# Performance work log

Hardware: AMD Instinct MI355X
Metric: run time of the kernel (lower is better)

Reference implementation:

```python
import jax, jax.numpy as jnp
import numpy as np

T, B, DIN, D = 512, 64, 1024, 1024


def setup_inputs() -> dict:
    key = jax.random.key(0)
    ks = jax.random.split(key, 11)
    s = 0.02
    inp = {
        "batch": jax.random.normal(ks[0], (T, B, DIN), dtype=jnp.float32),
        "lengths": jax.random.randint(ks[1], (B,), 0, T).astype(jnp.int32),
        "c0": jnp.zeros((D,), dtype=jnp.float32),
    }
    # gate weights stored [in, out] so application is x @ W + b
    for n, (kw, kb) in zip(["i", "f", "c", "o"], [(ks[2], ks[3]), (ks[4], ks[5]), (ks[6], ks[7]), (ks[8], ks[9])]):
        inp[f"W_{n}_w"] = jax.random.normal(kw, (DIN + D, D), dtype=jnp.float32) * s
        inp[f"W_{n}_b"] = jax.random.normal(kb, (D,), dtype=jnp.float32) * s
    return inp


def reference(batch, lengths, c0, W_i_w, W_i_b, W_f_w, W_f_b, W_c_w, W_c_b, W_o_w, W_o_b):
    Tn, Bn, _ = batch.shape
    c_init = jnp.broadcast_to(c0, (Bn, c0.shape[0]))
    h_init = jnp.tanh(c_init)
    # mask[t, b] = True where step t is past sequence b's length -> h zeroed
    mask = jnp.arange(Tn, dtype=lengths.dtype)[:, None] >= lengths[None, :]  # [T, B]

    def step(carry, xm):
        h, c = carry
        x_t, m_t = xm
        x = jnp.concatenate([x_t, h], axis=1)  # [B, DIN+D]
        i = jax.nn.sigmoid(x @ W_i_w + W_i_b)
        f = jax.nn.sigmoid(x @ W_f_w + W_f_b)
        g = jnp.tanh(x @ W_c_w + W_c_b)
        o = jax.nn.sigmoid(x @ W_o_w + W_o_b)
        c = f * c + i * g
        h = o * jnp.tanh(c)
        # in the original, new_output[mask]=0 mutates h in-place, so masked h
        # is carried into the next step's state as well as emitted as output
        h = jnp.where(m_t[:, None], jnp.zeros_like(h), h)
        return (h, c), h

    _, outs = jax.lax.scan(step, (h_init, c_init), (batch, mask))
    return outs  # [T, B, D]
```

## Files before the change

### kernel.cpp

```cpp
#include <hip/hip_runtime.h>
#include <cstddef>

typedef _Float16 f16;
typedef _Float16 f16x8 __attribute__((ext_vector_type(8)));
typedef _Float16 f16x4 __attribute__((ext_vector_type(4)));
typedef float f32x4 __attribute__((ext_vector_type(4)));

#define T_STEPS 512
#define BATCH   64
#define DD      1024
#define NTOT    4096


#define RSTRIDE_B 139264ull
#define RSTRIDE_H 69632ull
#define GSLAB_H   16384ull

#define OFF_FLAGS 0ull
#define OFF_BIAS  16384ull
#define OFF_WHP   32768ull
#define OFF_BXP   (OFF_WHP + 8388608ull)
#define OFF_XW    (OFF_BXP + 8388608ull)
#define XW_END    (OFF_XW + 268435456ull)
#define OFF_RING  XW_END
#define RING_END  (OFF_RING + 512ull * RSTRIDE_B)


__device__ __forceinline__ float sigm(float x) { return 1.f / (1.f + __expf(-x)); }
__device__ __forceinline__ float tanh_fast(float x) {
    float e = __expf(-2.f * fabsf(x));
    float t = (1.f - e) / (1.f + e);
    return x >= 0.f ? t : -t;
}

__device__ __forceinline__ unsigned int load_coh_u32(const unsigned int* p) {
    return __hip_atomic_load((unsigned int*)p, __ATOMIC_RELAXED, __HIP_MEMORY_SCOPE_AGENT);
}
__device__ __forceinline__ void store_coh_u32(unsigned int* p, unsigned int v) {
    __hip_atomic_store(p, v, __ATOMIC_RELAXED, __HIP_MEMORY_SCOPE_AGENT);
}
__device__ __forceinline__ void store_coh_u64(unsigned long long* p, unsigned long long v) {
    __hip_atomic_store(p, v, __ATOMIC_RELAXED, __HIP_MEMORY_SCOPE_AGENT);
}
__device__ __forceinline__ void waitcnt_vm0() {
    asm volatile("s_waitcnt vmcnt(0)" ::: "memory");
}

#define GATE4(g4, x0, x1, x2, x3, cvar, hvar)                        \
    {                                                                \
        float pi = (g4).x + (float)(x0);                             \
        float pf = (g4).y + (float)(x1);                             \
        float pg = (g4).z + (float)(x2);                             \
        float po = (g4).w + (float)(x3);                             \
        float iv = sigm(pi), fv = sigm(pf);                          \
        float gg = tanh_fast(pg), ov = sigm(po);                     \
        cvar = fv * cvar + iv * gg;                                  \
        hvar = ov * tanh_fast(cvar);                                 \
    }

__global__ void prepack_kernel(const float* __restrict__ Wi, const float* __restrict__ Wf,
                               const float* __restrict__ Wc, const float* __restrict__ Wo,
                               const float* __restrict__ bi, const float* __restrict__ bf,
                               const float* __restrict__ bc, const float* __restrict__ bo,
                               const float* __restrict__ c0,
                               f16* __restrict__ whp, f16* __restrict__ bxp,
                               float* __restrict__ biasp, f16* __restrict__ ring0,
                               unsigned int* __restrict__ flags)
{
    unsigned int gid = blockIdx.x * 256u + threadIdx.x;
    if (gid < 4096u) flags[gid] = 0u;
    const float* Ww[4] = {Wi, Wf, Wc, Wo};
    if (gid < 8388608u) {
        unsigned int hi = (gid >= 4194304u);
        unsigned int e  = gid & 4194303u;
        unsigned int jj = e & 7u;
        unsigned int lidx = (e >> 3) & 63u;
        unsigned int S  = (e >> 9) & 31u;
        unsigned int NT = e >> 14;
        unsigned int n  = NT * 16u + (lidx & 15u);
        unsigned int k  = S * 32u + (lidx >> 4) * 8u + jj + (hi ? 1024u : 0u);
        unsigned int g  = n & 3u, d = n >> 2;
        float v = Ww[g][k * 1024u + d];
        (hi ? whp : bxp)[e] = (f16)v;
    } else if (gid < 8392704u) {
        unsigned int n = gid - 8388608u;
        const float* Bb[4] = {bi, bf, bc, bo};
        biasp[n] = Bb[n & 3u][n >> 2];
    } else if (gid < 8458240u) {
        unsigned int e2 = gid - 8392704u;
        ring0[e2] = (f16)tanh_fast(c0[e2 & 1023u]);
    }
}

__global__ __launch_bounds__(256) void gemm_x_kernel(
    const float* __restrict__ A, const f16* __restrict__ Bp,
    const float* __restrict__ biasp, f16* __restrict__ xw)
{
    const int tid = threadIdx.x;
    const int w = tid >> 6, l = tid & 63;
    const int lr = l & 15, lq = l >> 4;
    const int n0 = blockIdx.x * 128;
    const int m0 = blockIdx.y * 128;

    f32x4 acc[2][8];
#pragma unroll
    for (int mt = 0; mt < 2; mt++)
#pragma unroll
        for (int nt = 0; nt < 8; nt++) acc[mt][nt] = (f32x4){0.f, 0.f, 0.f, 0.f};

    const float* a0 = A + (size_t)(m0 + 32 * w + lr) * 1024 + lq * 8;
    const f16x8* bp = (const f16x8*)Bp + (size_t)(n0 >> 4) * (32 * 64) + l;

#pragma unroll 2
    for (int s = 0; s < 32; s++) {
        f16x8 af[2];
#pragma unroll
        for (int mt = 0; mt < 2; mt++) {
            const float* ap = a0 + mt * (16 * 1024) + 32 * s;
            float4 v0 = *(const float4*)ap;
            float4 v1 = *(const float4*)(ap + 4);
            f16x8 tt;
            tt[0] = (f16)v0.x; tt[1] = (f16)v0.y; tt[2] = (f16)v0.z; tt[3] = (f16)v0.w;
            tt[4] = (f16)v1.x; tt[5] = (f16)v1.y; tt[6] = (f16)v1.z; tt[7] = (f16)v1.w;
            af[mt] = tt;
        }
#pragma unroll
        for (int nt = 0; nt < 8; nt++) {
            f16x8 bfr = bp[(size_t)(nt * 32 + s) * 64];
            acc[0][nt] = __builtin_amdgcn_mfma_f32_16x16x32_f16(af[0], bfr, acc[0][nt], 0, 0, 0);
            acc[1][nt] = __builtin_amdgcn_mfma_f32_16x16x32_f16(af[1], bfr, acc[1][nt], 0, 0, 0);
        }
    }
#pragma unroll
    for (int nt = 0; nt < 8; nt++) {
        int n = n0 + nt * 16 + lr;
        float bias = biasp[n];
#pragma unroll
        for (int mt = 0; mt < 2; mt++) {
#pragma unroll
            for (int r = 0; r < 4; r++) {
                int m = m0 + 32 * w + mt * 16 + lq * 4 + r;
                xw[(size_t)m * NTOT + n] = (f16)(acc[mt][nt][r] + bias);
            }
        }
    }
}

__global__ __launch_bounds__(256, 1) void lstm_persist_ring(
    const f16* __restrict__ xw, const f16* __restrict__ whp,
    const int* __restrict__ lengths, const float* __restrict__ c0,
    float* __restrict__ out, f16* ring, unsigned int* flags)
{
    extern __shared__ __align__(16) char smem[];
    f16*   wlds    = (f16*)smem;
    float* pre_lds = (float*)(smem + 131072);

    const int g  = blockIdx.x & 3;
    const int j2 = blockIdx.x >> 2;
    const int tid = threadIdx.x;
    const int wv = tid >> 6, l = tid & 63;
    const int lr = l & 15, lq = l >> 4;

    {
        const f16x8* wp = (const f16x8*)whp + (size_t)(4 * j2) * 2048;
        f16x8* wl0 = (f16x8*)wlds;
        for (int i = tid; i < 8192; i += 256) wl0[i] = wp[i];
    }
    __syncthreads();

    const int koff = lq * 8;
    const f16x8* wl = (const f16x8*)wlds + wv * 2048 + l;

    unsigned int* myflag = flags + (unsigned int)g * 1024u + (unsigned int)j2 * 16u;
    unsigned int* gflags = flags + (unsigned int)g * 1024u;

    const int b_local = tid >> 2, q = tid & 3;
    const int b_glob  = 16 * g + b_local;
    float cA = 0.f, cB = 0.f, cC = 0.f, cD = 0.f;
    int len = 0;
    const f16* xwbase = nullptr;
    f16x8 xg0 = (f16x8)0, xg1 = (f16x8)0;
    if (tid < 64) {
        float4 ci = *(const float4*)&c0[16 * j2 + 4 * q];
        cA = ci.x; cB = ci.y; cC = ci.z; cD = ci.w;
        len = lengths[b_glob];
        xwbase = xw + (size_t)b_glob * NTOT + 64 * j2 + 16 * q;
        xg0 = *(const f16x8*)xwbase;
        xg1 = *(const f16x8*)(xwbase + 8);
    }

    const size_t slab = (size_t)g * GSLAB_H;

    for (int t = 0; t < T_STEPS; t++) {
        const f16* hb = ring + (size_t)t * RSTRIDE_H + slab;
        const f16x8* ap = (const f16x8*)(hb + (size_t)lr * DD + koff);

        f16x8 xg0n = xg0, xg1n = xg1;
        if (tid < 64 && t + 1 < T_STEPS) {
            const f16* nx = xwbase + (size_t)(t + 1) * (BATCH * NTOT);
            xg0n = *(const f16x8*)nx;
            xg1n = *(const f16x8*)(nx + 8);
        }

        f32x4 acc0 = {0.f, 0.f, 0.f, 0.f}, acc1 = {0.f, 0.f, 0.f, 0.f};
#pragma unroll
        for (int s = 0; s < 32; s += 2) {
            f16x8 a0 = ap[4 * s];
            f16x8 a1 = ap[4 * (s + 1)];
            f16x8 w0 = wl[64 * s];
            f16x8 w1 = wl[64 * (s + 1)];
            acc0 = __builtin_amdgcn_mfma_f32_16x16x32_f16(a0, w0, acc0, 0, 0, 0);
            acc1 = __builtin_amdgcn_mfma_f32_16x16x32_f16(a1, w1, acc1, 0, 0, 0);
        }
        f32x4 pre = acc0 + acc1;
#pragma unroll
        for (int r = 0; r < 4; r++)
            pre_lds[(lq * 4 + r) * 68 + 16 * wv + lr] = pre[r];
        __syncthreads();

        float4 oh = (float4){0.f, 0.f, 0.f, 0.f};
        if (tid < 64) {
            const float* pr = &pre_lds[b_local * 68 + 16 * q];
            float4 g0 = *(const float4*)(pr + 0);
            float4 g1 = *(const float4*)(pr + 4);
            float4 g2 = *(const float4*)(pr + 8);
            float4 g3 = *(const float4*)(pr + 12);
            float h0, h1, h2, h3;
            GATE4(g0, xg0[0], xg0[1], xg0[2], xg0[3], cA, h0);
            GATE4(g1, xg0[4], xg0[5], xg0[6], xg0[7], cB, h1);
            GATE4(g2, xg1[0], xg1[1], xg1[2], xg1[3], cC, h2);
            GATE4(g3, xg1[4], xg1[5], xg1[6], xg1[7], cD, h3);
            if (t >= len) { h0 = 0.f; h1 = 0.f; h2 = 0.f; h3 = 0.f; }
            oh = (float4){h0, h1, h2, h3};
            if (t + 1 < T_STEPS) {
                f16x4 hv;
                hv[0] = (f16)h0; hv[1] = (f16)h1; hv[2] = (f16)h2; hv[3] = (f16)h3;
                store_coh_u64((unsigned long long*)(ring + (size_t)(t + 1) * RSTRIDE_H + slab
                                                    + (size_t)b_local * DD + 16 * j2 + 4 * q),
                              __builtin_bit_cast(unsigned long long, hv));
            }
        }

        if (t + 1 < T_STEPS) {
            waitcnt_vm0();
            __syncthreads();
            if (tid == 0) store_coh_u32(myflag, (unsigned int)(t + 1));
            if (tid < 64)
                *(float4*)(out + (size_t)t * (BATCH * DD) + (size_t)b_glob * DD
                           + 16 * j2 + 4 * q) = oh;
            if (wv == 0) {
                const unsigned int want = (unsigned int)(t + 1);
                while (!__all(load_coh_u32(gflags + 16 * l) >= want))
                    __builtin_amdgcn_s_sleep(1);
            }
            __syncthreads();
            asm volatile("" ::: "memory");
        } else {
            if (tid < 64)
                *(float4*)(out + (size_t)t * (BATCH * DD) + (size_t)b_glob * DD
                           + 16 * j2 + 4 * q) = oh;
        }
        xg0 = xg0n; xg1 = xg1n;
    }
}

extern "C" void kernel_launch(void* const* d_in, const int* in_sizes, int n_in,
                              void* d_out, int out_size, void* d_ws, size_t ws_size,
                              hipStream_t stream) {
    const float* batch   = (const float*)d_in[0];
    const int*   lengths = (const int*)d_in[1];
    const float* c0      = (const float*)d_in[2];
    const float* Wi = (const float*)d_in[3];
    const float* bi = (const float*)d_in[4];
    const float* Wf = (const float*)d_in[5];
    const float* bf = (const float*)d_in[6];
    const float* Wc = (const float*)d_in[7];
    const float* bc = (const float*)d_in[8];
    const float* Wo = (const float*)d_in[9];
    const float* bo = (const float*)d_in[10];
    float* out = (float*)d_out;

    char* ws = (char*)d_ws;
    unsigned int* flags = (unsigned int*)(ws + OFF_FLAGS);
    float* biasp = (float*)(ws + OFF_BIAS);
    f16*   whp   = (f16*)(ws + OFF_WHP);
    f16*   bxp   = (f16*)(ws + OFF_BXP);
    f16*   xw    = (f16*)(ws + OFF_XW);
    f16*   ring  = (f16*)(ws + OFF_RING);

    prepack_kernel<<<33040, 256, 0, stream>>>(Wi, Wf, Wc, Wo, bi, bf, bc, bo, c0,
                                              whp, bxp, biasp, ring, flags);
    gemm_x_kernel<<<dim3(32, 256), 256, 0, stream>>>(batch, bxp, biasp, xw);
    lstm_persist_ring<<<256, 256, 135424, stream>>>(xw, whp, lengths, c0, out, ring, flags);
}
```

Before: 4.125 ms.

## Replace per-step global barrier with per-chunk flag polling overlapped with MFMA

Each wave now waits only for the 16 producer blocks that own the K-chunk it is about to consume. It issues the h loads for a chunk before polling the next chunk's flags, so dependency waits overlap with the recurrent matmul instead of a full-group barrier at the end of each step. The pre-activation LDS buffer is double-buffered by step parity, which lets the trailing __syncthreads be dropped. The trade-off is that all four waves poll global flags, which raises coherent-load traffic and needs slightly more shared memory.

```diff
diff --git a/kernel.cpp b/kernel.cpp
--- a/kernel.cpp
+++ b/kernel.cpp
@@ -172,7 +172,7 @@
     const f16x8* wl = (const f16x8*)wlds + wv * 2048 + l;
 
     unsigned int* myflag = flags + (unsigned int)g * 1024u + (unsigned int)j2 * 16u;
-    unsigned int* gflags = flags + (unsigned int)g * 1024u;
+    const unsigned int* pollp = flags + (unsigned int)g * 1024u + (unsigned int)(l & 15) * 16u;
 
     const int b_local = tid >> 2, q = tid & 3;
     const int b_glob  = 16 * g + b_local;
@@ -202,25 +202,45 @@
             xg1n = *(const f16x8*)(nx + 8);
         }
 
+        const unsigned int want = (unsigned int)t;
         f32x4 acc0 = {0.f, 0.f, 0.f, 0.f}, acc1 = {0.f, 0.f, 0.f, 0.f};
-#pragma unroll
-        for (int s = 0; s < 32; s += 2) {
-            f16x8 a0 = ap[4 * s];
-            f16x8 a1 = ap[4 * (s + 1)];
-            f16x8 w0 = wl[64 * s];
-            f16x8 w1 = wl[64 * (s + 1)];
-            acc0 = __builtin_amdgcn_mfma_f32_16x16x32_f16(a0, w0, acc0, 0, 0, 0);
-            acc1 = __builtin_amdgcn_mfma_f32_16x16x32_f16(a1, w1, acc1, 0, 0, 0);
+
+        if (t > 0) {
+            while (!__all(load_coh_u32(pollp + 0 * 256) >= want))
+                __builtin_amdgcn_s_sleep(1);
+            asm volatile("" ::: "memory");
+        }
+
+#pragma unroll
+        for (int c = 0; c < 4; c++) {
+            f16x8 a[8];
+            const f16x8* apc = ap + 32 * c;
+#pragma unroll
+            for (int i = 0; i < 8; i++) a[i] = apc[4 * i];
+
+            if (t > 0 && c < 3) {
+                while (!__all(load_coh_u32(pollp + (c + 1) * 256) >= want))
+                    __builtin_amdgcn_s_sleep(1);
+                asm volatile("" ::: "memory");
+            }
+
+            const f16x8* wlc = wl + 64 * (8 * c);
+#pragma unroll
+            for (int i = 0; i < 8; i += 2) {
+                acc0 = __builtin_amdgcn_mfma_f32_16x16x32_f16(a[i],     wlc[64 * i],       acc0, 0, 0, 0);
+                acc1 = __builtin_amdgcn_mfma_f32_16x16x32_f16(a[i + 1], wlc[64 * (i + 1)], acc1, 0, 0, 0);
+            }
         }
         f32x4 pre = acc0 + acc1;
+
+        float* pb = pre_lds + (size_t)(t & 1) * (16 * 68);
 #pragma unroll
         for (int r = 0; r < 4; r++)
-            pre_lds[(lq * 4 + r) * 68 + 16 * wv + lr] = pre[r];
+            pb[(lq * 4 + r) * 68 + 16 * wv + lr] = pre[r];
         __syncthreads();
 
-        float4 oh = (float4){0.f, 0.f, 0.f, 0.f};
         if (tid < 64) {
-            const float* pr = &pre_lds[b_local * 68 + 16 * q];
+            const float* pr = &pb[b_local * 68 + 16 * q];
             float4 g0 = *(const float4*)(pr + 0);
             float4 g1 = *(const float4*)(pr + 4);
             float4 g2 = *(const float4*)(pr + 8);
@@ -231,34 +251,17 @@
             GATE4(g2, xg1[0], xg1[1], xg1[2], xg1[3], cC, h2);
             GATE4(g3, xg1[4], xg1[5], xg1[6], xg1[7], cD, h3);
             if (t >= len) { h0 = 0.f; h1 = 0.f; h2 = 0.f; h3 = 0.f; }
-            oh = (float4){h0, h1, h2, h3};
             if (t + 1 < T_STEPS) {
                 f16x4 hv;
                 hv[0] = (f16)h0; hv[1] = (f16)h1; hv[2] = (f16)h2; hv[3] = (f16)h3;
                 store_coh_u64((unsigned long long*)(ring + (size_t)(t + 1) * RSTRIDE_H + slab
                                                     + (size_t)b_local * DD + 16 * j2 + 4 * q),
                               __builtin_bit_cast(unsigned long long, hv));
-            }
-        }
-
-        if (t + 1 < T_STEPS) {
-            waitcnt_vm0();
-            __syncthreads();
-            if (tid == 0) store_coh_u32(myflag, (unsigned int)(t + 1));
-            if (tid < 64)
-                *(float4*)(out + (size_t)t * (BATCH * DD) + (size_t)b_glob * DD
-                           + 16 * j2 + 4 * q) = oh;
-            if (wv == 0) {
-                const unsigned int want = (unsigned int)(t + 1);
-                while (!__all(load_coh_u32(gflags + 16 * l) >= want))
-                    __builtin_amdgcn_s_sleep(1);
-            }
-            __syncthreads();
-            asm volatile("" ::: "memory");
-        } else {
-            if (tid < 64)
-                *(float4*)(out + (size_t)t * (BATCH * DD) + (size_t)b_glob * DD
-                           + 16 * j2 + 4 * q) = oh;
+                waitcnt_vm0();
+                if (tid == 0) store_coh_u32(myflag, (unsigned int)(t + 1));
+            }
+            *(float4*)(out + (size_t)t * (BATCH * DD) + (size_t)b_glob * DD
+                       + 16 * j2 + 4 * q) = (float4){h0, h1, h2, h3};
         }
         xg0 = xg0n; xg1 = xg1n;
     }
@@ -291,5 +294,5 @@
     prepack_kernel<<<33040, 256, 0, stream>>>(Wi, Wf, Wc, Wo, bi, bf, bc, bo, c0,
                                               whp, bxp, biasp, ring, flags);
     gemm_x_kernel<<<dim3(32, 256), 256, 0, stream>>>(batch, bxp, biasp, xw);
-    lstm_persist_ring<<<256, 256, 135424, stream>>>(xw, whp, lengths, c0, out, ring, flags);
-}
+    lstm_persist_ring<<<256, 256, 139776, stream>>>(xw, whp, lengths, c0, out, ring, flags);
+}
```

Result: slower. 4.368 ms (+5.9%).
